# Performance work log

Measured on AMD Instinct MI355X. Metric: run time of the kernel, lower is better.

The kernel has to match this reference:

```python
import jax, jax.numpy as jnp
import numpy as np

ETA = 3.0       # eta_px
KCAP = 96       # k_pos_cap
POS_W = 1.2     # obj_pos_weight
LCD = 1.0       # lambda_cd
LP0 = 1.0       # lambda_p0


def setup_inputs() -> dict:
    key = jax.random.key(0)
    k1, k2, k3, k4, k5, k6 = jax.random.split(key, 6)
    B, H, W, Ng, C = 4, 192, 192, 64, 4
    img = 192 * 8.0
    ctr = jax.random.uniform(k4, (B, Ng, 1, 2), minval=60.0, maxval=img - 60.0)
    offs = jax.random.normal(k5, (B, Ng, 3, 2)) * 30.0
    return {
        "pred_reg": jax.random.normal(k1, (B, 6, H, W), dtype=jnp.float32),
        "pred_obj": jax.random.normal(k2, (B, 1, H, W), dtype=jnp.float32),
        "pred_cls": jax.random.normal(k3, (B, C, H, W), dtype=jnp.float32),
        "gt_pts": (ctr + offs).astype(jnp.float32),
        "gt_lbl": jax.random.randint(k6, (B, Ng), 0, C),
        "stride": 8,
    }


def _loss_core(pred_reg, pred_obj, pred_cls, gt_pts, gt_lbl, stride):
    B, _, H, W = pred_reg.shape
    N = H * W
    C = pred_cls.shape[1]
    s = jnp.float32(stride)
    ys = (jnp.arange(H, dtype=jnp.float32) + 0.5) * s
    xs = (jnp.arange(W, dtype=jnp.float32) + 0.5) * s
    yy, xx = jnp.meshgrid(ys, xs, indexing='ij')
    px = xx.reshape(N)  # grid-center x, [N]
    py = yy.reshape(N)

    A = gt_pts[:, :, 0, :]   # [B,Ng,2]
    Bv = gt_pts[:, :, 1, :]
    Cv = gt_pts[:, :, 2, :]

    def sgn(P, Q):  # sign test of cell center vs edge (P,Q); broadcasts to [B,Ng,N]
        return (px - Q[..., 0:1]) * (P[..., 1:2] - Q[..., 1:2]) - (P[..., 0:1] - Q[..., 0:1]) * (py - Q[..., 1:2])

    d1 = sgn(A, Bv); d2 = sgn(Bv, Cv); d3 = sgn(Cv, A)
    has_neg = (d1 < 0) | (d2 < 0) | (d3 < 0)
    has_pos = (d1 > 0) | (d2 > 0) | (d3 > 0)
    inside = ~(has_neg & has_pos)  # [B,Ng,N]

    def seg(P, Q):  # point-to-segment distance, [B,Ng,N]
        vx = Q[..., 0:1] - P[..., 0:1]
        vy = Q[..., 1:2] - P[..., 1:2]
        wx = px - P[..., 0:1]
        wy = py - P[..., 1:2]
        t = jnp.clip((wx * vx + wy * vy) / (vx * vx + vy * vy + 1e-9), 0.0, 1.0)
        dx = wx - t * vx
        dy = wy - t * vy
        return jnp.sqrt(dx * dx + dy * dy + 1e-12)

    dist = jnp.minimum(seg(A, Bv), jnp.minimum(seg(Bv, Cv), seg(Cv, A)))  # [B,Ng,N]
    pos = inside | (dist <= ETA)

    # top-k cap: keep the KCAP closest positive cells per GT (matches torch topk(-d))
    dmask = jnp.where(pos, dist, jnp.inf)
    negv, idx = jax.lax.top_k(-dmask, KCAP)  # [B,Ng,KCAP]
    valid = jnp.isfinite(negv)               # True only for actual positives
    capped = jax.vmap(jax.vmap(lambda i, v: jnp.zeros((N,), bool).at[i].set(v)))(idx, valid)  # [B,Ng,N]

    # objectness BCE-with-logits with pos_weight, summed
    obj_t = capped.any(axis=1).astype(pred_obj.dtype)  # [B,N]
    x = pred_obj.reshape(B, N)
    obj_loss = jnp.sum(-(POS_W * obj_t * jax.nn.log_sigmoid(x) + (1.0 - obj_t) * jax.nn.log_sigmoid(-x)))

    # class targets: nearest GT (by triangle distance) among capped positives
    dcls = jnp.where(capped, dist, jnp.inf)
    jbest = jnp.argmin(dcls, axis=1)                   # [B,N]; first index on ties, like sequential strict <
    cellmask = jnp.isfinite(jnp.min(dcls, axis=1))     # [B,N]
    tgt = jnp.take_along_axis(gt_lbl, jbest, axis=1)   # [B,N]
    logits = pred_cls.reshape(B, C, N).transpose(0, 2, 1)  # [B,N,C]
    lse = jax.nn.logsumexp(logits, axis=-1)
    picked = jnp.take_along_axis(logits, tgt[..., None], axis=-1)[..., 0]
    cls_loss = jnp.sum(jnp.where(cellmask, lse - picked, 0.0))

    centers_flat = jnp.stack([px, py], axis=-1)        # [N,2]
    anchors = centers_flat[idx]                        # [B,Ng,K,2]
    pred_off = pred_reg.transpose(0, 2, 3, 1).reshape(B, N, 3, 2)
    pred_sel = jax.vmap(lambda p, i: p[i])(pred_off, idx)          # [B,Ng,K,3,2]
    gt_off = (gt_pts[:, :, None, :, :] - anchors[:, :, :, None, :]) / s  # [B,Ng,K,3,2]
    w = valid.astype(pred_reg.dtype)                   # [B,Ng,K]

    loss_p0 = jnp.sum(w * jnp.sum((pred_sel[..., 0, :] - gt_off[..., 0, :]) ** 2, axis=-1))
    # chamfer between the 2 tail points; original: chamfer_2pts(...) * npix == per-cell (d1+d2) summed
    dmat = jnp.sqrt(jnp.sum((pred_sel[:, :, :, 1:, None, :] - gt_off[:, :, :, None, 1:, :]) ** 2, axis=-1) + 1e-12)  # [B,Ng,K,2,2]
    cd = jnp.sum(w * (dmat.min(axis=-1).sum(axis=-1) + dmat.min(axis=-2).sum(axis=-1)))
    reg_loss = LP0 * loss_p0 + LCD * cd

    return jnp.stack([reg_loss, obj_loss, cls_loss])


def reference(pred_reg, pred_obj, pred_cls, gt_pts, gt_lbl, stride):
    return _loss_core(pred_reg, pred_obj, pred_cls, gt_pts, gt_lbl, stride)
```

## Files before the change

### kernel.cpp

```cpp
#include <hip/hip_runtime.h>
#include <stdint.h>

#define ETA    3.0f
#define KCAP   96
#define POS_W  1.2f
#define NG     64
#define BATCH  4
#define HH     192
#define WW     192
#define NCELL  (HH*WW)
#define NCLS   4
#define CAP    4096
#define PTHR   256
#define NWAVE  4
#define NBLK   (BATCH*NG)
#define SEGS   16
#define NB2    (BATCH*SEGS)
#define SEGC   (NCELL/SEGS)
#define BCLAIM (NG*KCAP)
#define INF64  0xFFFFFFFFFFFFFFFFull
#define TOPBIT 0x8000000000000000ull

#define WS_CCNT_OFF   16
#define WS_CLAIM_OFF  (WS_CCNT_OFF + NBLK*4)
#define WS_PA_OFF     (WS_CLAIM_OFF + NBLK*KCAP*8)
#define WS_PC_OFF     (WS_PA_OFF + NBLK*16)

#define OBJ4_PER_BLK 144

__device__ __forceinline__ float log_sigmoid(float x) {
    return fminf(x, 0.0f) - __logf(1.0f + __expf(-fabsf(x)));
}

__device__ __forceinline__ float segsq(float wx, float wy, float vx, float vy, float inv) {
    float t = (wx * vx + wy * vy) * inv;
    t = fminf(fmaxf(t, 0.0f), 1.0f);
    float dx = wx - t * vx;
    float dy = wy - t * vy;
    return dx * dx + dy * dy;
}

__device__ __forceinline__ void block_red5(float v[5], float* sbuf) {
    #pragma unroll
    for (int off = 32; off > 0; off >>= 1) {
        #pragma unroll
        for (int q = 0; q < 5; ++q) v[q] += __shfl_down(v[q], off);
    }
    const int lane = threadIdx.x & 63;
    const int wid  = threadIdx.x >> 6;
    __syncthreads();
    if (lane == 0) {
        #pragma unroll
        for (int q = 0; q < 5; ++q) sbuf[wid * 5 + q] = v[q];
    }
    __syncthreads();
    if (threadIdx.x == 0) {
        #pragma unroll
        for (int q = 0; q < 5; ++q) {
            float r = 0.0f;
            #pragma unroll
            for (int w = 0; w < NWAVE; ++w) r += sbuf[w * 5 + q];
            v[q] = r;
        }
    }
}

__global__ __launch_bounds__(PTHR)
void pair_kernel(const float* __restrict__ pred_reg,
                 const float* __restrict__ pred_obj,
                 const float* __restrict__ gt_pts,
                 const int*   __restrict__ stride_p,
                 int* __restrict__ ccnt,
                 unsigned long long* __restrict__ claims,
                 float4* __restrict__ pA,
                 int* __restrict__ arrival)
{
    const int pair = blockIdx.x;
    const int b    = pair >> 6;
    const int tid  = threadIdx.x;
    const int lane = tid & 63;
    const int wid  = tid >> 6;
    const float s  = (float)(*stride_p);

    __shared__ unsigned long long keys[CAP];
    __shared__ int   hist[PTHR];
    __shared__ float sbuf[NWAVE * 5];
    __shared__ int   wsum[NWAVE];
    __shared__ int   scnt, ccl, sd, sp;

    if (pair == 0 && tid == 0) *arrival = 0;

    float c_obj = 0.0f;
    if (tid < OBJ4_PER_BLK) {
        const float4 v = ((const float4*)pred_obj)[pair * OBJ4_PER_BLK + tid];
        c_obj = -log_sigmoid(-v.x) - log_sigmoid(-v.y)
                - log_sigmoid(-v.z) - log_sigmoid(-v.w);
    }

    const float* gp = gt_pts + (size_t)pair * 6;
    const float Ax = gp[0], Ay = gp[1];
    const float Bx = gp[2], By = gp[3];
    const float Cx = gp[4], Cy = gp[5];

    const float vABx = Bx - Ax, vABy = By - Ay;
    const float vBCx = Cx - Bx, vBCy = Cy - By;
    const float vCAx = Ax - Cx, vCAy = Ay - Cy;
    const float invAB = 1.0f / (vABx * vABx + vABy * vABy + 1e-9f);
    const float invBC = 1.0f / (vBCx * vBCx + vBCy * vBCy + 1e-9f);
    const float invCA = 1.0f / (vCAx * vCAx + vCAy * vCAy + 1e-9f);

    const float xmin = fminf(Ax, fminf(Bx, Cx)) - ETA;
    const float xmax = fmaxf(Ax, fmaxf(Bx, Cx)) + ETA;
    const float ymin = fminf(Ay, fminf(By, Cy)) - ETA;
    const float ymax = fmaxf(Ay, fmaxf(By, Cy)) + ETA;
    const float inv_sf = 1.0f / s;
    int j0 = max(0,      (int)floorf(xmin * inv_sf - 0.5f) - 1);
    int j1 = min(WW - 1, (int)ceilf (xmax * inv_sf - 0.5f) + 1);
    int i0 = max(0,      (int)floorf(ymin * inv_sf - 0.5f) - 1);
    int i1 = min(HH - 1, (int)ceilf (ymax * inv_sf - 0.5f) + 1);
    const int nbw = j1 - j0 + 1;
    const int nbh = i1 - i0 + 1;
    const int nb  = (nbw > 0 && nbh > 0) ? nbw * nbh : 0;

    if (tid == 0) { scnt = 0; ccl = 0; }
    __syncthreads();

    for (int t = tid; t < nb; t += PTHR) {
        const int li = t / nbw;
        const int lj = t - li * nbw;
        const int i = i0 + li;
        const int j = j0 + lj;
        const float px = ((float)j + 0.5f) * s;
        const float py = ((float)i + 0.5f) * s;

        const float d1 = (px - Bx) * (Ay - By) - (Ax - Bx) * (py - By);
        const float d2 = (px - Cx) * (By - Cy) - (Bx - Cx) * (py - Cy);
        const float d3 = (px - Ax) * (Cy - Ay) - (Cx - Ax) * (py - Ay);
        const bool has_neg = (d1 < 0.0f) | (d2 < 0.0f) | (d3 < 0.0f);
        const bool has_pos = (d1 > 0.0f) | (d2 > 0.0f) | (d3 > 0.0f);
        const bool inside = !(has_neg && has_pos);

        float dsq = segsq(px - Ax, py - Ay, vABx, vABy, invAB);
        dsq = fminf(dsq, segsq(px - Bx, py - By, vBCx, vBCy, invBC));
        dsq = fminf(dsq, segsq(px - Cx, py - Cy, vCAx, vCAy, invCA));
        const float dist = sqrtf(dsq + 1e-12f);

        if (inside || dist <= ETA) {
            int slot = atomicAdd(&scnt, 1);
            if (slot < CAP) {
                const int n = i * WW + j;
                keys[slot] = (((unsigned long long)__float_as_uint(dist)) << 16) | (unsigned)n;
            }
        }
    }
    __syncthreads();

    const int M = min(scnt, CAP);
    unsigned long long T = INF64;

    if (M > KCAP) {
        unsigned long long prefix = 0;
        int need = KCAP;
        for (int shift = 40; shift >= 0; shift -= 8) {
            hist[tid] = 0;
            __syncthreads();
            for (int t = tid; t < M; t += PTHR) {
                const unsigned long long k = keys[t];
                if ((k >> (shift + 8)) == prefix)
                    atomicAdd(&hist[(int)((k >> shift) & 0xFF)], 1);
            }
            __syncthreads();
            const int h = hist[tid];
            int incl = h;
            #pragma unroll
            for (int off = 1; off < 64; off <<= 1) {
                const int o = __shfl_up(incl, off);
                if (lane >= off) incl += o;
            }
            if (lane == 63) wsum[wid] = incl;
            __syncthreads();
            #pragma unroll
            for (int w = 0; w < NWAVE; ++w) if (w < wid) incl += wsum[w];
            const int excl = incl - h;
            if (excl < need && incl >= need) { sd = tid; sp = excl; }
            __syncthreads();
            prefix = (prefix << 8) | (unsigned)sd;
            need  -= sp;
            __syncthreads();
        }
        T = prefix;
    }

    float c_reg = 0.0f;
    for (int t = tid; t < M; t += PTHR) {
        const unsigned long long k = keys[t];
        if (k > T) continue;
        const int n = (int)(k & 0xFFFFull);

        const int slot = atomicAdd(&ccl, 1);
        if (slot < KCAP)
            claims[(size_t)pair * KCAP + slot] =
                ((k >> 16) << 32) | (unsigned long long)(unsigned)n;

        const int i = n / WW;
        const int j = n - i * WW;
        const float ax = ((float)j + 0.5f) * s;
        const float ay = ((float)i + 0.5f) * s;

        const float g0x = (Ax - ax) * inv_sf, g0y = (Ay - ay) * inv_sf;
        const float g1x = (Bx - ax) * inv_sf, g1y = (By - ay) * inv_sf;
        const float g2x = (Cx - ax) * inv_sf, g2y = (Cy - ay) * inv_sf;

        const float* pr = pred_reg + (size_t)b * 6 * NCELL + n;
        const float p0x = pr[0 * NCELL], p0y = pr[1 * NCELL];
        const float p1x = pr[2 * NCELL], p1y = pr[3 * NCELL];
        const float p2x = pr[4 * NCELL], p2y = pr[5 * NCELL];

        c_reg += (p0x - g0x) * (p0x - g0x) + (p0y - g0y) * (p0y - g0y);

        const float d11 = sqrtf((p1x - g1x) * (p1x - g1x) + (p1y - g1y) * (p1y - g1y) + 1e-12f);
        const float d12 = sqrtf((p1x - g2x) * (p1x - g2x) + (p1y - g2y) * (p1y - g2y) + 1e-12f);
        const float d21 = sqrtf((p2x - g1x) * (p2x - g1x) + (p2y - g1y) * (p2y - g1y) + 1e-12f);
        const float d22 = sqrtf((p2x - g2x) * (p2x - g2x) + (p2y - g2y) * (p2y - g2y) + 1e-12f);

        c_reg += fminf(d11, d12) + fminf(d21, d22)
               + fminf(d11, d21) + fminf(d12, d22);
    }
    __syncthreads();
    if (tid == 0) ccnt[pair] = min(ccl, KCAP);

    float v[5] = { c_reg, c_obj, 0.0f, 0.0f, 0.0f };
    block_red5(v, sbuf);
    if (tid == 0) pA[pair] = make_float4(v[0], v[1], 0.0f, 0.0f);
}

__global__ __launch_bounds__(PTHR)
void resolve_kernel(const float* __restrict__ pred_obj,
                    const float* __restrict__ pred_cls,
                    const int*   __restrict__ gt_lbl,
                    const int*   __restrict__ ccnt,
                    const unsigned long long* __restrict__ claims,
                    const float4* __restrict__ pA,
                    float4* __restrict__ pC,
                    int* __restrict__ arrival,
                    float* __restrict__ out)
{
    const int blk = blockIdx.x;
    const int b   = blk >> 4;
    const int seg = blk & (SEGS - 1);
    const int n0  = seg * SEGC;
    const int tid = threadIdx.x;

    __shared__ unsigned int       table[SEGC];
    __shared__ unsigned long long cl[BCLAIM];
    __shared__ int   cnts[NG];
    __shared__ float sbuf[NWAVE * 5];
    __shared__ int   ccl, islast;

    if (tid < NG) cnts[tid] = ccnt[b * NG + tid];
    if (tid == 0) { ccl = 0; islast = 0; }
    for (int i = tid; i < SEGC; i += PTHR) table[i] = 0xFFFFFFFFu;
    __syncthreads();

    const unsigned long long* bcl = claims + (size_t)b * BCLAIM;
    for (int sIdx = tid; sIdx < BCLAIM; sIdx += PTHR) {
        const int pg = sIdx / KCAP;
        const int r  = sIdx - pg * KCAP;
        if (r < cnts[pg]) {
            const unsigned long long e = bcl[sIdx];
            const int ln = (int)(e & 0xFFFFull) - n0;
            if ((unsigned)ln < (unsigned)SEGC) {
                const int i = atomicAdd(&ccl, 1);
                cl[i] = e | ((unsigned long long)pg << 16);
                atomicMin(&table[ln], (unsigned)(e >> 32));
            }
        }
    }
    __syncthreads();
    const int NC = ccl;

    for (int i = tid; i < NC; i += PTHR) {
        const unsigned long long e = cl[i];
        const int ln = (int)(e & 0xFFFFull) - n0;
        if (table[ln] == (unsigned)(e >> 32)) cl[i] = e | TOPBIT;
    }
    __syncthreads();
    for (int i = tid; i < NC; i += PTHR) {
        const unsigned long long e = cl[i];
        if (e & TOPBIT) {
            const int ln = (int)(e & 0xFFFFull) - n0;
            atomicMin(&table[ln], (unsigned)((e >> 16) & 63ull));
        }
    }
    __syncthreads();

    float v[5] = { 0.0f, 0.0f, 0.0f, 0.0f, 0.0f };
    const size_t bc = (size_t)b * NCLS * NCELL;
    for (int i = tid; i < NC; i += PTHR) {
        const unsigned long long e = cl[i];
        if (!(e & TOPBIT)) continue;
        const int n = (int)(e & 0xFFFFull);
        const int g = (int)((e >> 16) & 63ull);
        if (table[n - n0] != (unsigned)g) continue;

        const float x = pred_obj[b * NCELL + n];
        v[0] += (-POS_W * log_sigmoid(x)) + log_sigmoid(-x);

        const float* pc = pred_cls + bc + n;
        const float l0 = pc[0];
        const float l1 = pc[NCELL];
        const float l2 = pc[2 * NCELL];
        const float l3 = pc[3 * NCELL];
        const float m = fmaxf(fmaxf(l0, l1), fmaxf(l2, l3));
        v[1] += m + __logf(__expf(l0 - m) + __expf(l1 - m)
                         + __expf(l2 - m) + __expf(l3 - m));
        const int tgt = gt_lbl[b * NG + g];
        v[2] += (tgt == 0) ? l0 : (tgt == 1) ? l1 : (tgt == 2) ? l2 : l3;
    }
    block_red5(v, sbuf);

    if (tid == 0) {
        pC[blk] = make_float4(v[0], v[1], v[2], 0.0f);
        __threadfence();
        const int old = atomicAdd(arrival, 1);
        if (old == NB2 - 1) islast = 1;
    }
    __syncthreads();
    if (!islast) return;
    __threadfence();

    const float4 a = pA[tid];
    const float4 c = (tid < NB2) ? pC[tid] : make_float4(0.f, 0.f, 0.f, 0.f);
    float w[5] = { a.x, a.y, c.x, c.y, c.z };
    block_red5(w, sbuf);
    if (tid == 0) {
        out[0] = w[0];
        out[1] = w[1] + w[2];
        out[2] = w[3] - w[4];
    }
}

extern "C" void kernel_launch(void* const* d_in, const int* in_sizes, int n_in,
                              void* d_out, int out_size, void* d_ws, size_t ws_size,
                              hipStream_t stream) {
    const float* pred_reg = (const float*)d_in[0];
    const float* pred_obj = (const float*)d_in[1];
    const float* pred_cls = (const float*)d_in[2];
    const float* gt_pts   = (const float*)d_in[3];
    const int*   gt_lbl   = (const int*)d_in[4];
    const int*   stride_p = (const int*)d_in[5];
    float* out = (float*)d_out;

    char* ws = (char*)d_ws;
    int* arrival = (int*)ws;
    int* ccnt    = (int*)(ws + WS_CCNT_OFF);
    unsigned long long* claims = (unsigned long long*)(ws + WS_CLAIM_OFF);
    float4* pA = (float4*)(ws + WS_PA_OFF);
    float4* pC = (float4*)(ws + WS_PC_OFF);

    (void)in_sizes; (void)n_in; (void)ws_size; (void)out_size;

    hipLaunchKernelGGL(pair_kernel, dim3(NBLK), dim3(PTHR), 0, stream,
                       pred_reg, pred_obj, gt_pts, stride_p,
                       ccnt, claims, pA, arrival);
    hipLaunchKernelGGL(resolve_kernel, dim3(NB2), dim3(PTHR), 0, stream,
                       pred_obj, pred_cls, gt_lbl, ccnt, claims, pA,
                       pC, arrival, out);
}
```

Baseline: 22.25 us.

## Fuse pair and resolve kernels into one launch with flag-based inter-block sync

Merges the two kernel launches into a single kernel. Per-pair completion flags in workspace let the first 16 blocks of each batch spin-wait on the batch's pair blocks before running the resolve phase. Block 0 then waits for all resolve flags, does the final reduction and clears the flags for the next call. This removes the second launch and its inter-kernel gap, but it relies on all 256 blocks being co-resident (otherwise it deadlocks) and the union-sized shared memory may reduce occupancy.

```diff
diff --git a/kernel.cpp b/kernel.cpp
--- a/kernel.cpp
+++ b/kernel.cpp
@@ -20,11 +20,14 @@
 #define BCLAIM (NG*KCAP)
 #define INF64  0xFFFFFFFFFFFFFFFFull
 #define TOPBIT 0x8000000000000000ull
-
-#define WS_CCNT_OFF   16
-#define WS_CLAIM_OFF  (WS_CCNT_OFF + NBLK*4)
-#define WS_PA_OFF     (WS_CLAIM_OFF + NBLK*KCAP*8)
-#define WS_PC_OFF     (WS_PA_OFF + NBLK*16)
+#define FSET   0x5EC0DE5Au
+
+#define WS_PDONE 0
+#define WS_RDONE 1024
+#define WS_CCNT  1280
+#define WS_PA    2304
+#define WS_PC    6400
+#define WS_CLAIM 7424
 
 #define OBJ4_PER_BLK 144
 
@@ -38,6 +41,13 @@
     float dx = wx - t * vx;
     float dy = wy - t * vy;
     return dx * dx + dy * dy;
+}
+
+__device__ __forceinline__ unsigned aload(const unsigned* p) {
+    return __hip_atomic_load(p, __ATOMIC_RELAXED, __HIP_MEMORY_SCOPE_AGENT);
+}
+__device__ __forceinline__ void astore(unsigned* p, unsigned v) {
+    __hip_atomic_store(p, v, __ATOMIC_RELAXED, __HIP_MEMORY_SCOPE_AGENT);
 }
 
 __device__ __forceinline__ void block_red5(float v[5], float* sbuf) {
@@ -66,14 +76,16 @@
 }
 
 __global__ __launch_bounds__(PTHR)
-void pair_kernel(const float* __restrict__ pred_reg,
-                 const float* __restrict__ pred_obj,
-                 const float* __restrict__ gt_pts,
-                 const int*   __restrict__ stride_p,
-                 int* __restrict__ ccnt,
-                 unsigned long long* __restrict__ claims,
-                 float4* __restrict__ pA,
-                 int* __restrict__ arrival)
+void fused_kernel(const float* __restrict__ pred_reg,
+                  const float* __restrict__ pred_obj,
+                  const float* __restrict__ pred_cls,
+                  const float* __restrict__ gt_pts,
+                  const int*   __restrict__ gt_lbl,
+                  const int*   __restrict__ stride_p,
+                  unsigned* pdone, unsigned* rdone, unsigned* ccnt_g,
+                  float4* pA, float4* pC,
+                  unsigned long long* claims,
+                  float* out)
 {
     const int pair = blockIdx.x;
     const int b    = pair >> 6;
@@ -82,13 +94,13 @@
     const int wid  = tid >> 6;
     const float s  = (float)(*stride_p);
 
-    __shared__ unsigned long long keys[CAP];
-    __shared__ int   hist[PTHR];
+    __shared__ union {
+        struct { unsigned long long keys[CAP]; int hist[PTHR]; } p;
+        struct { unsigned long long cl[BCLAIM]; unsigned table[SEGC]; int cnts[NG]; } r;
+    } U;
     __shared__ float sbuf[NWAVE * 5];
     __shared__ int   wsum[NWAVE];
     __shared__ int   scnt, ccl, sd, sp;
-
-    if (pair == 0 && tid == 0) *arrival = 0;
 
     float c_obj = 0.0f;
     if (tid < OBJ4_PER_BLK) {
@@ -149,7 +161,7 @@
             int slot = atomicAdd(&scnt, 1);
             if (slot < CAP) {
                 const int n = i * WW + j;
-                keys[slot] = (((unsigned long long)__float_as_uint(dist)) << 16) | (unsigned)n;
+                U.p.keys[slot] = (((unsigned long long)__float_as_uint(dist)) << 16) | (unsigned)n;
             }
         }
     }
@@ -162,15 +174,15 @@
         unsigned long long prefix = 0;
         int need = KCAP;
         for (int shift = 40; shift >= 0; shift -= 8) {
-            hist[tid] = 0;
+            U.p.hist[tid] = 0;
             __syncthreads();
             for (int t = tid; t < M; t += PTHR) {
-                const unsigned long long k = keys[t];
+                const unsigned long long k = U.p.keys[t];
                 if ((k >> (shift + 8)) == prefix)
-                    atomicAdd(&hist[(int)((k >> shift) & 0xFF)], 1);
-            }
-            __syncthreads();
-            const int h = hist[tid];
+                    atomicAdd(&U.p.hist[(int)((k >> shift) & 0xFF)], 1);
+            }
+            __syncthreads();
+            const int h = U.p.hist[tid];
             int incl = h;
             #pragma unroll
             for (int off = 1; off < 64; off <<= 1) {
@@ -193,7 +205,7 @@
 
     float c_reg = 0.0f;
     for (int t = tid; t < M; t += PTHR) {
-        const unsigned long long k = keys[t];
+        const unsigned long long k = U.p.keys[t];
         if (k > T) continue;
         const int n = (int)(k & 0xFFFFull);
 
@@ -227,116 +239,127 @@
                + fminf(d11, d21) + fminf(d12, d22);
     }
     __syncthreads();
-    if (tid == 0) ccnt[pair] = min(ccl, KCAP);
-
-    float v[5] = { c_reg, c_obj, 0.0f, 0.0f, 0.0f };
-    block_red5(v, sbuf);
-    if (tid == 0) pA[pair] = make_float4(v[0], v[1], 0.0f, 0.0f);
-}
-
-__global__ __launch_bounds__(PTHR)
-void resolve_kernel(const float* __restrict__ pred_obj,
-                    const float* __restrict__ pred_cls,
-                    const int*   __restrict__ gt_lbl,
-                    const int*   __restrict__ ccnt,
-                    const unsigned long long* __restrict__ claims,
-                    const float4* __restrict__ pA,
-                    float4* __restrict__ pC,
-                    int* __restrict__ arrival,
-                    float* __restrict__ out)
-{
-    const int blk = blockIdx.x;
-    const int b   = blk >> 4;
-    const int seg = blk & (SEGS - 1);
-    const int n0  = seg * SEGC;
-    const int tid = threadIdx.x;
-
-    __shared__ unsigned int       table[SEGC];
-    __shared__ unsigned long long cl[BCLAIM];
-    __shared__ int   cnts[NG];
-    __shared__ float sbuf[NWAVE * 5];
-    __shared__ int   ccl, islast;
-
-    if (tid < NG) cnts[tid] = ccnt[b * NG + tid];
-    if (tid == 0) { ccl = 0; islast = 0; }
-    for (int i = tid; i < SEGC; i += PTHR) table[i] = 0xFFFFFFFFu;
-    __syncthreads();
-
-    const unsigned long long* bcl = claims + (size_t)b * BCLAIM;
-    for (int sIdx = tid; sIdx < BCLAIM; sIdx += PTHR) {
-        const int pg = sIdx / KCAP;
-        const int r  = sIdx - pg * KCAP;
-        if (r < cnts[pg]) {
-            const unsigned long long e = bcl[sIdx];
+    if (tid == 0) ccnt_g[pair] = (unsigned)min(ccl, KCAP);
+
+    {
+        float v5[5] = { c_reg, c_obj, 0.0f, 0.0f, 0.0f };
+        block_red5(v5, sbuf);
+        if (tid == 0) {
+            pA[pair] = make_float4(v5[0], v5[1], 0.0f, 0.0f);
+            __threadfence();
+            astore(&pdone[pair], FSET);
+        }
+    }
+
+    if ((pair & 63) < SEGS) {
+        const int seg = pair & 63;
+        const int n0  = seg * SEGC;
+
+        __syncthreads();
+
+        if (wid == 0) {
+            for (;;) {
+                const unsigned f = aload(&pdone[(b << 6) + lane]);
+                if (__all(f == FSET)) break;
+                __builtin_amdgcn_s_sleep(2);
+            }
+        }
+        __syncthreads();
+        __threadfence();
+
+        if (tid < NG) U.r.cnts[tid] = (int)ccnt_g[(b << 6) + tid];
+        for (int i = tid; i < SEGC; i += PTHR) U.r.table[i] = 0xFFFFFFFFu;
+        if (tid == 0) ccl = 0;
+        __syncthreads();
+
+        const unsigned long long* bcl = claims + (size_t)b * BCLAIM;
+        for (int sIdx = tid; sIdx < BCLAIM; sIdx += PTHR) {
+            const int pg = sIdx / KCAP;
+            const int r  = sIdx - pg * KCAP;
+            if (r < U.r.cnts[pg]) {
+                const unsigned long long e = bcl[sIdx];
+                const int ln = (int)(e & 0xFFFFull) - n0;
+                if ((unsigned)ln < (unsigned)SEGC) {
+                    const int i = atomicAdd(&ccl, 1);
+                    U.r.cl[i] = e | ((unsigned long long)pg << 16);
+                    atomicMin(&U.r.table[ln], (unsigned)(e >> 32));
+                }
+            }
+        }
+        __syncthreads();
+        const int NC = ccl;
+
+        for (int i = tid; i < NC; i += PTHR) {
+            const unsigned long long e = U.r.cl[i];
             const int ln = (int)(e & 0xFFFFull) - n0;
-            if ((unsigned)ln < (unsigned)SEGC) {
-                const int i = atomicAdd(&ccl, 1);
-                cl[i] = e | ((unsigned long long)pg << 16);
-                atomicMin(&table[ln], (unsigned)(e >> 32));
-            }
-        }
-    }
-    __syncthreads();
-    const int NC = ccl;
-
-    for (int i = tid; i < NC; i += PTHR) {
-        const unsigned long long e = cl[i];
-        const int ln = (int)(e & 0xFFFFull) - n0;
-        if (table[ln] == (unsigned)(e >> 32)) cl[i] = e | TOPBIT;
-    }
-    __syncthreads();
-    for (int i = tid; i < NC; i += PTHR) {
-        const unsigned long long e = cl[i];
-        if (e & TOPBIT) {
-            const int ln = (int)(e & 0xFFFFull) - n0;
-            atomicMin(&table[ln], (unsigned)((e >> 16) & 63ull));
-        }
-    }
-    __syncthreads();
-
-    float v[5] = { 0.0f, 0.0f, 0.0f, 0.0f, 0.0f };
-    const size_t bc = (size_t)b * NCLS * NCELL;
-    for (int i = tid; i < NC; i += PTHR) {
-        const unsigned long long e = cl[i];
-        if (!(e & TOPBIT)) continue;
-        const int n = (int)(e & 0xFFFFull);
-        const int g = (int)((e >> 16) & 63ull);
-        if (table[n - n0] != (unsigned)g) continue;
-
-        const float x = pred_obj[b * NCELL + n];
-        v[0] += (-POS_W * log_sigmoid(x)) + log_sigmoid(-x);
-
-        const float* pc = pred_cls + bc + n;
-        const float l0 = pc[0];
-        const float l1 = pc[NCELL];
-        const float l2 = pc[2 * NCELL];
-        const float l3 = pc[3 * NCELL];
-        const float m = fmaxf(fmaxf(l0, l1), fmaxf(l2, l3));
-        v[1] += m + __logf(__expf(l0 - m) + __expf(l1 - m)
-                         + __expf(l2 - m) + __expf(l3 - m));
-        const int tgt = gt_lbl[b * NG + g];
-        v[2] += (tgt == 0) ? l0 : (tgt == 1) ? l1 : (tgt == 2) ? l2 : l3;
-    }
-    block_red5(v, sbuf);
-
-    if (tid == 0) {
-        pC[blk] = make_float4(v[0], v[1], v[2], 0.0f);
-        __threadfence();
-        const int old = atomicAdd(arrival, 1);
-        if (old == NB2 - 1) islast = 1;
-    }
-    __syncthreads();
-    if (!islast) return;
-    __threadfence();
-
-    const float4 a = pA[tid];
-    const float4 c = (tid < NB2) ? pC[tid] : make_float4(0.f, 0.f, 0.f, 0.f);
-    float w[5] = { a.x, a.y, c.x, c.y, c.z };
-    block_red5(w, sbuf);
-    if (tid == 0) {
-        out[0] = w[0];
-        out[1] = w[1] + w[2];
-        out[2] = w[3] - w[4];
+            if (U.r.table[ln] == (unsigned)(e >> 32)) U.r.cl[i] = e | TOPBIT;
+        }
+        __syncthreads();
+        for (int i = tid; i < NC; i += PTHR) {
+            const unsigned long long e = U.r.cl[i];
+            if (e & TOPBIT) {
+                const int ln = (int)(e & 0xFFFFull) - n0;
+                atomicMin(&U.r.table[ln], (unsigned)((e >> 16) & 63ull));
+            }
+        }
+        __syncthreads();
+
+        float v[5] = { 0.0f, 0.0f, 0.0f, 0.0f, 0.0f };
+        const size_t bc = (size_t)b * NCLS * NCELL;
+        for (int i = tid; i < NC; i += PTHR) {
+            const unsigned long long e = U.r.cl[i];
+            if (!(e & TOPBIT)) continue;
+            const int n = (int)(e & 0xFFFFull);
+            const int g = (int)((e >> 16) & 63ull);
+            if (U.r.table[n - n0] != (unsigned)g) continue;
+
+            const float x = pred_obj[b * NCELL + n];
+            v[0] += (-POS_W * log_sigmoid(x)) + log_sigmoid(-x);
+
+            const float* pc = pred_cls + bc + n;
+            const float l0 = pc[0];
+            const float l1 = pc[NCELL];
+            const float l2 = pc[2 * NCELL];
+            const float l3 = pc[3 * NCELL];
+            const float m = fmaxf(fmaxf(l0, l1), fmaxf(l2, l3));
+            v[1] += m + __logf(__expf(l0 - m) + __expf(l1 - m)
+                             + __expf(l2 - m) + __expf(l3 - m));
+            const int tgt = gt_lbl[b * NG + g];
+            v[2] += (tgt == 0) ? l0 : (tgt == 1) ? l1 : (tgt == 2) ? l2 : l3;
+        }
+        block_red5(v, sbuf);
+        if (tid == 0) {
+            pC[(b << 4) + seg] = make_float4(v[0], v[1], v[2], 0.0f);
+            __threadfence();
+            astore(&rdone[(b << 4) + seg], FSET);
+        }
+
+        if (pair == 0) {
+            __syncthreads();
+            if (wid == 0) {
+                for (;;) {
+                    const unsigned f = aload(&rdone[lane]);
+                    if (__all(f == FSET)) break;
+                    __builtin_amdgcn_s_sleep(2);
+                }
+            }
+            __syncthreads();
+            __threadfence();
+
+            const float4 a = pA[tid];
+            float4 c = make_float4(0.f, 0.f, 0.f, 0.f);
+            if (tid < NB2) c = pC[tid];
+            float w5[5] = { a.x, a.y, c.x, c.y, c.z };
+            block_red5(w5, sbuf);
+            if (tid == 0) {
+                out[0] = w5[0];
+                out[1] = w5[1] + w5[2];
+                out[2] = w5[3] - w5[4];
+            }
+
+            if (tid < NBLK) astore(&pdone[tid], 0u);
+            if (tid < NB2)  astore(&rdone[tid], 0u);
+        }
     }
 }
 
@@ -352,18 +375,16 @@
     float* out = (float*)d_out;
 
     char* ws = (char*)d_ws;
-    int* arrival = (int*)ws;
-    int* ccnt    = (int*)(ws + WS_CCNT_OFF);
-    unsigned long long* claims = (unsigned long long*)(ws + WS_CLAIM_OFF);
-    float4* pA = (float4*)(ws + WS_PA_OFF);
-    float4* pC = (float4*)(ws + WS_PC_OFF);
+    unsigned* pdone = (unsigned*)(ws + WS_PDONE);
+    unsigned* rdone = (unsigned*)(ws + WS_RDONE);
+    unsigned* ccnt  = (unsigned*)(ws + WS_CCNT);
+    float4*   pA    = (float4*)(ws + WS_PA);
+    float4*   pC    = (float4*)(ws + WS_PC);
+    unsigned long long* claims = (unsigned long long*)(ws + WS_CLAIM);
 
     (void)in_sizes; (void)n_in; (void)ws_size; (void)out_size;
 
-    hipLaunchKernelGGL(pair_kernel, dim3(NBLK), dim3(PTHR), 0, stream,
-                       pred_reg, pred_obj, gt_pts, stride_p,
-                       ccnt, claims, pA, arrival);
-    hipLaunchKernelGGL(resolve_kernel, dim3(NB2), dim3(PTHR), 0, stream,
-                       pred_obj, pred_cls, gt_lbl, ccnt, claims, pA,
-                       pC, arrival, out);
-}
+    hipLaunchKernelGGL(fused_kernel, dim3(NBLK), dim3(PTHR), 0, stream,
+                       pred_reg, pred_obj, pred_cls, gt_pts, gt_lbl, stride_p,
+                       pdone, rdone, ccnt, pA, pC, claims, out);
+}
```

Result: slower. 28.79 us (+29.4%).
